# Optimization experiments

Measured on AMD Instinct MI355X. Metric: run time of the kernel, lower is better.

## Reference

```python
import jax, jax.numpy as jnp
import numpy as np

B, S, H = 256, 1024, 256  # batch, seq_len, hidden(==input_size)


def setup_inputs() -> dict:
    key = jax.random.key(0)
    ks = jax.random.split(key, 7)
    s = 1.0 / np.sqrt(H).astype(np.float32)
    return {
        "x": jax.random.normal(ks[0], (B, S, H), jnp.float32),
        "h_n": jax.random.normal(ks[1], (1, B, H), jnp.float32),
        "c_n": jax.random.normal(ks[2], (1, B, H), jnp.float32),
        "W_ih": jax.random.uniform(ks[3], (4 * H, H), jnp.float32, -s, s),
        "W_hh": jax.random.uniform(ks[4], (4 * H, H), jnp.float32, -s, s),
        "b_ih": jax.random.uniform(ks[5], (4 * H,), jnp.float32, -s, s),
        "b_hh": jax.random.uniform(ks[6], (4 * H,), jnp.float32, -s, s),
    }


def _lstm_decode(x, h_n, c_n, W_ih, W_hh, b_ih, b_hh):
    # Original torch loop: step 0 consumes h_n as the input token, step i>=1
    # consumes x[:, i-1]; outputs[:, i] is the hidden state after step i.
    h0, c0 = h_n[0], c_n[0]                               # (B, H)
    seq_in = jnp.concatenate([h0[:, None, :], x[:, :-1, :]], axis=1)  # (B, S, H)
    # Precompute input projections for the whole sequence (gate order i,f,g,o).
    x_proj = jnp.einsum("bsd,gd->bsg", seq_in, W_ih) + (b_ih + b_hh)   # (B, S, 4H)
    x_proj = jnp.swapaxes(x_proj, 0, 1)                   # (S, B, 4H)

    def step(carry, xp):
        h, c = carry
        gates = xp + h @ W_hh.T                           # (B, 4H)
        i, f, g, o = jnp.split(gates, 4, axis=-1)
        c = jax.nn.sigmoid(f) * c + jax.nn.sigmoid(i) * jnp.tanh(g)
        h = jax.nn.sigmoid(o) * jnp.tanh(c)
        return (h, c), h

    _, hs = jax.lax.scan(step, (h0, c0), x_proj)          # hs: (S, B, H)
    return jnp.swapaxes(hs, 0, 1)                         # (B, S, H)


def reference(x, h_n, c_n, W_ih, W_hh, b_ih, b_hh):
    return _lstm_decode(x, h_n, c_n, W_ih, W_hh, b_ih, b_hh)
```

## Files before the change

### kernel.cpp

```cpp
#include <hip/hip_runtime.h>
#include <stdint.h>


using bf16x8 = __attribute__((ext_vector_type(8))) __bf16;
using f32x4  = __attribute__((ext_vector_type(4))) float;
using u32x4  = __attribute__((ext_vector_type(4))) uint32_t;
using u16x2  = __attribute__((ext_vector_type(2))) uint16_t;

#define NCHUNK 8

#define XS_OFF   0ull
#define XS_SZ    134217728ull
#define WIH_OFF  (XS_OFF + XS_SZ)
#define W_SZ     524288ull
#define WHH_OFF  (WIH_OFF + W_SZ)
#define XP0_OFF  (WHH_OFF + W_SZ)
#define XP_SZ    67108864ull
#define XP1_OFF  (XP0_OFF + XP_SZ)
#define HST_OFF  (XP1_OFF + XP_SZ)
#define HST_SZ   131072ull
#define CST_OFF  (HST_OFF + HST_SZ)
#define CST_SZ   262144ull
#define BIAS_OFF (CST_OFF + CST_SZ)

#define WLDS_PER_WAVE 18432
#define HOFF   147456
#define LDS_BYTES 163840

#define SC_IFO -1.442695041f
#define SC_G   -2.885390082f

__device__ __forceinline__ uint16_t f2bf(float f) {
  uint32_t x = __float_as_uint(f);
  x += 0x7fffu + ((x >> 16) & 1u);
  return (uint16_t)(x >> 16);
}
__device__ __forceinline__ float bf2f(uint16_t u) {
  return __uint_as_float(((uint32_t)u) << 16);
}
__device__ __forceinline__ float frcp(float x) { return __builtin_amdgcn_rcpf(x); }
__device__ __forceinline__ float exp2a(float x) {
  float r; asm("v_exp_f32 %0, %1" : "=v"(r) : "v"(x)); return r;
}

__device__ __forceinline__ f32x4 mfma16(u32x4 a, u32x4 b, f32x4 c) {
  return __builtin_amdgcn_mfma_f32_16x16x32_bf16(
      __builtin_bit_cast(bf16x8, a), __builtin_bit_cast(bf16x8, b), c, 0, 0, 0);
}

#define W_IN_REG(f, kt) ((kt) < 5 || ((kt) == 5 && (f) < 6))
#define WIDX(f, kt)     ((f) < 6 ? (f) * 6 + (kt) : 36 + ((f) - 6) * 5 + (kt))
#define LIDX(f, kt)     ((kt) == 5 ? ((f) - 6) : ((kt) == 6 ? 2 + (f) : 10 + (f)))

__global__ __launch_bounds__(256) void pack_x_k(const float* __restrict__ x,
                                                const float* __restrict__ hn,
                                                uint16_t* __restrict__ xsp) {
  __shared__ uint16_t tile[64 * 256];
  const int t = blockIdx.x;
  const int tid = threadIdx.x;
  for (int pass = 0; pass < 2; ++pass) {
    const int r = tid >> 2;
    const int qq = tid & 3;
    const int rg = t * 128 + pass * 64 + r;
    const int s = rg >> 8, b = rg & 255;
    const float* src = s ? (x + ((size_t)b * 1024 + (s - 1)) * 256)
                         : (hn + (size_t)b * 256);
#pragma unroll
    for (int i = 0; i < 64; i += 2) {
      float2 v = *(const float2*)(src + qq * 64 + i);
      uint32_t kb = (uint32_t)(qq * 64 + i) * 2u;
      uint32_t addr = (uint32_t)r * 512u + (kb ^ (((uint32_t)r & 7u) << 4));
      u16x2 pr; pr.x = f2bf(v.x); pr.y = f2bf(v.y);
      *(u16x2*)((char*)tile + addr) = pr;
    }
    __syncthreads();
#pragma unroll
    for (int ff = 0; ff < 8; ++ff) {
      int task = ff * 256 + tid;
      int frag = task >> 6, lam = task & 63;
      int mt = frag >> 3, kt = frag & 7;
      int row = mt * 16 + (lam & 15);
      uint32_t kb = (uint32_t)(kt * 64 + (lam >> 4) * 16);
      u32x4 d = *(const u32x4*)((const char*)tile + row * 512 +
                                (kb ^ (((uint32_t)row & 7u) << 4)));
      size_t m16 = (size_t)t * 8 + pass * 4 + mt;
      *(u32x4*)(xsp + ((m16 * 8 + kt) * 64 + lam) * 8) = d;
    }
    __syncthreads();
  }
}

__global__ __launch_bounds__(256) void pack_misc_k(
    const float* __restrict__ wih, const float* __restrict__ whh,
    const float* __restrict__ bih, const float* __restrict__ bhh,
    const float* __restrict__ hn, const float* __restrict__ cn,
    uint16_t* __restrict__ wihp, uint16_t* __restrict__ whhp,
    float* __restrict__ bias, uint16_t* __restrict__ hst, float* __restrict__ cst) {
  const int blk = blockIdx.x, tid = threadIdx.x;
  if (blk < 32) {
    __shared__ uint16_t tile[64 * 256];
    const float* W = (blk < 16) ? wih : whh;
    uint16_t* WP = (blk < 16) ? wihp : whhp;
    const int rowbase = (blk & 15) * 64;
    const int r = tid >> 2, qq = tid & 3;
    const int n = rowbase + r;
    const float sc = ((n >> 8) == 2) ? SC_G : SC_IFO;
    const float* src = W + (size_t)n * 256;
#pragma unroll
    for (int i = 0; i < 64; i += 2) {
      float2 v = *(const float2*)(src + qq * 64 + i);
      uint32_t kb = (uint32_t)(qq * 64 + i) * 2u;
      uint32_t addr = (uint32_t)r * 512u + (kb ^ (((uint32_t)r & 7u) << 4));
      u16x2 pr; pr.x = f2bf(v.x * sc); pr.y = f2bf(v.y * sc);
      *(u16x2*)((char*)tile + addr) = pr;
    }
    __syncthreads();
#pragma unroll
    for (int ff = 0; ff < 8; ++ff) {
      int task = ff * 256 + tid;
      int frag = task >> 6, lam = task & 63;
      int mt = frag >> 3, kt = frag & 7;
      int row = mt * 16 + (lam & 15);
      uint32_t kb = (uint32_t)(kt * 64 + (lam >> 4) * 16);
      u32x4 d = *(const u32x4*)((const char*)tile + row * 512 +
                                (kb ^ (((uint32_t)row & 7u) << 4)));
      size_t nt = (size_t)(blk & 15) * 4 + mt;
      *(u32x4*)(WP + ((nt * 8 + kt) * 64 + lam) * 8) = d;
    }
  } else if (blk == 32) {
    for (int i = tid; i < 4096; i += 256) {
      float sc = ((i >> 8) == 2) ? SC_G : SC_IFO;
      bias[i] = (bih[i] + bhh[i]) * sc;
    }
  } else if (blk == 33) {
    for (int it = 0; it < 32; ++it) {
      int task = it * 256 + tid;
      int lam = task & 63;
      int kt = (task >> 6) & 7;
      int lb = task >> 9;
      int b = lb * 16 + (lam & 15);
      int k0 = kt * 32 + (lam >> 4) * 8;
      union { uint16_t s[8]; u32x4 v; } u;
#pragma unroll
      for (int j = 0; j < 8; ++j) u.s[j] = f2bf(hn[(size_t)b * 256 + k0 + j]);
      *(u32x4*)(hst + (size_t)task * 8) = u.v;
    }
  } else {
    for (int it = 0; it < 16; ++it) {
      int lt = it * 512 + (blk - 34) * 256 + tid;
      int l = lt & 63;
      int w = (lt >> 6) & 7;
      int lb = lt >> 9;
#pragma unroll
      for (int v = 0; v < 8; ++v) {
        int q = v & 3, hs = v >> 2;
        int bb = lb * 16 + (l >> 4) * 4 + q;
        int j = w * 32 + hs * 16 + (l & 15);
        cst[(size_t)lt * 8 + v] = cn[(size_t)bb * 256 + j];
      }
    }
  }
}

__global__ __launch_bounds__(512, 1) void fused_k(
    const uint16_t* __restrict__ xsp, const uint16_t* __restrict__ wihp,
    const uint16_t* __restrict__ whhp, const float* __restrict__ bias,
    uint16_t* __restrict__ xp0, uint16_t* __restrict__ xp1,
    uint16_t* __restrict__ hst, float* __restrict__ cst,
    float* __restrict__ out, int lstm_chunk, int gemm_chunk) {
  extern __shared__ __align__(16) char lds[];
  const int tid = threadIdx.x;
  const int l = tid & 63;
  const int w = tid >> 6;

  if (blockIdx.x < 16) {
    if (lstm_chunk < 0) return;
    const int c = lstm_chunk;
    const int blk = blockIdx.x;
    const uint16_t* __restrict__ xp = (c & 1) ? xp1 : xp0;

    u32x4 wr[46];
#pragma unroll
    for (int f = 0; f < 8; ++f) {
#pragma unroll
      for (int kt = 0; kt < 8; ++kt) {
        int nt = (f & 3) * 16 + (w * 2 + (f >> 2));
        u32x4 d = *(const u32x4*)(whhp + (((size_t)nt * 8 + kt) * 64 + l) * 8);
        if (W_IN_REG(f, kt))
          wr[WIDX(f, kt)] = d;
        else
          *(u32x4*)(lds + w * WLDS_PER_WAVE + LIDX(f, kt) * 1024 + l * 16) = d;
      }
    }
    *(u32x4*)(lds + HOFF + tid * 16) =
        *(const u32x4*)(hst + (size_t)blk * 4096 + (size_t)tid * 8);
    float creg[8];
    {
      const float* cs = cst + ((size_t)(blk * 8 + w) * 64 + l) * 8;
#pragma unroll
      for (int v = 0; v < 8; ++v) creg[v] = cs[v];
    }
    const char* xpbase = (const char*)xp +
        ((((size_t)blk * 128) * 16 + (size_t)(w * 2)) * 64 + l) * 32;
    float* ob = out + ((size_t)(blk * 16 + (l >> 4) * 4) * 1024 + (size_t)c * 128) * 256 + (l & 15);
    __syncthreads();

    int p = 0;
#pragma unroll 1
    for (int s = 0; s < 128; ++s) {
      const char* xc = xpbase + (size_t)s * 32768;
      union XV { uint16_t sv[16]; u32x4 v[2]; };
      XV xv0;
      xv0.v[0] = *(const u32x4*)(xc);
      xv0.v[1] = *(const u32x4*)(xc + 16);
      const char* hb = lds + HOFF + p * 8192 + l * 16;
      char* hw = lds + HOFF + (p ^ 1) * 8192;

      f32x4 acc0[4] = {};
#pragma unroll
      for (int kt = 0; kt < 8; ++kt) {
        u32x4 a = *(const u32x4*)(hb + kt * 1024);
#pragma unroll
        for (int g = 0; g < 4; ++g) {
          u32x4 b = W_IN_REG(g, kt)
                        ? wr[WIDX(g, kt)]
                        : *(const u32x4*)(lds + w * WLDS_PER_WAVE + LIDX(g, kt) * 1024 + l * 16);
          acc0[g] = mfma16(a, b, acc0[g]);
        }
      }
      XV xv1;
      xv1.v[0] = *(const u32x4*)(xc + 2048);
      xv1.v[1] = *(const u32x4*)(xc + 2048 + 16);
      {
        const int j = (w * 2) * 16 + (l & 15);
        char* hwj = hw + (j >> 5) * 1024 + (((j >> 3) & 3) * 16) * 16 + (j & 7) * 2;
        float* obh = ob + (size_t)s * 256 + (w * 2) * 16;
#pragma unroll
        for (int q = 0; q < 4; ++q) {
          float xi = acc0[0][q] + bf2f(xv0.sv[0 * 4 + q]);
          float xf = acc0[1][q] + bf2f(xv0.sv[1 * 4 + q]);
          float xg = acc0[2][q] + bf2f(xv0.sv[2 * 4 + q]);
          float xo = acc0[3][q] + bf2f(xv0.sv[3 * 4 + q]);
          float I = frcp(1.f + exp2a(xi));
          float F = frcp(1.f + exp2a(xf));
          float T = fmaf(2.f, frcp(1.f + exp2a(xg)), -1.f);
          float O = frcp(1.f + exp2a(xo));
          float cv = fmaf(F, creg[q], I * T);
          creg[q] = cv;
          float th = fmaf(2.f, frcp(1.f + exp2a(SC_G * cv)), -1.f);
          float hv = O * th;
          obh[(size_t)q * 262144] = hv;
          int m = (l >> 4) * 4 + q;
          *(uint16_t*)(hwj + m * 16) = f2bf(hv);
        }
      }

      f32x4 acc1[4] = {};
#pragma unroll
      for (int kt = 0; kt < 8; ++kt) {
        u32x4 a = *(const u32x4*)(hb + kt * 1024);
#pragma unroll
        for (int g = 0; g < 4; ++g) {
          u32x4 b = W_IN_REG(4 + g, kt)
                        ? wr[WIDX(4 + g, kt)]
                        : *(const u32x4*)(lds + w * WLDS_PER_WAVE + LIDX(4 + g, kt) * 1024 + l * 16);
          acc1[g] = mfma16(a, b, acc1[g]);
        }
      }
      {
        const int j = (w * 2 + 1) * 16 + (l & 15);
        char* hwj = hw + (j >> 5) * 1024 + (((j >> 3) & 3) * 16) * 16 + (j & 7) * 2;
        float* obh = ob + (size_t)s * 256 + (w * 2 + 1) * 16;
#pragma unroll
        for (int q = 0; q < 4; ++q) {
          float xi = acc1[0][q] + bf2f(xv1.sv[0 * 4 + q]);
          float xf = acc1[1][q] + bf2f(xv1.sv[1 * 4 + q]);
          float xg = acc1[2][q] + bf2f(xv1.sv[2 * 4 + q]);
          float xo = acc1[3][q] + bf2f(xv1.sv[3 * 4 + q]);
          float I = frcp(1.f + exp2a(xi));
          float F = frcp(1.f + exp2a(xf));
          float T = fmaf(2.f, frcp(1.f + exp2a(xg)), -1.f);
          float O = frcp(1.f + exp2a(xo));
          float cv = fmaf(F, creg[4 + q], I * T);
          creg[4 + q] = cv;
          float th = fmaf(2.f, frcp(1.f + exp2a(SC_G * cv)), -1.f);
          float hv = O * th;
          obh[(size_t)q * 262144] = hv;
          int m = (l >> 4) * 4 + q;
          *(uint16_t*)(hwj + m * 16) = f2bf(hv);
        }
      }
      __syncthreads();
      p ^= 1;
    }
    *(u32x4*)(hst + (size_t)blk * 4096 + (size_t)tid * 8) =
        *(const u32x4*)(lds + HOFF + p * 8192 + tid * 16);
    {
      float* cs = cst + ((size_t)(blk * 8 + w) * 64 + l) * 8;
#pragma unroll
      for (int v = 0; v < 8; ++v) cs[v] = creg[v];
    }
    return;
  }

  if (gemm_chunk < 0) return;
  const int c = gemm_chunk;
  const int bid = blockIdx.x - 16;
  const int sg = bid >> 4;
  const int bb = bid & 15;

  f32x4 acc[4][2][4] = {};
#pragma unroll
  for (int kt = 0; kt < 8; ++kt) {
    u32x4 av[4];
#pragma unroll
    for (int mt = 0; mt < 4; ++mt) {
      size_t m16 = (size_t)(c * 128 + sg * 4 + mt) * 16 + bb;
      av[mt] = *(const u32x4*)(xsp + ((m16 * 8 + kt) * 64 + l) * 8);
    }
    u32x4 bv[2][4];
#pragma unroll
    for (int jj = 0; jj < 2; ++jj)
#pragma unroll
      for (int g = 0; g < 4; ++g) {
        size_t nt = (size_t)(g * 16 + w * 2 + jj);
        bv[jj][g] = *(const u32x4*)(wihp + ((nt * 8 + kt) * 64 + l) * 8);
      }
#pragma unroll
    for (int mt = 0; mt < 4; ++mt)
#pragma unroll
      for (int jj = 0; jj < 2; ++jj)
#pragma unroll
        for (int g = 0; g < 4; ++g)
          acc[mt][jj][g] = mfma16(av[mt], bv[jj][g], acc[mt][jj][g]);
  }
  uint16_t* __restrict__ xpo = (c & 1) ? xp1 : xp0;
  float badd[2][4];
#pragma unroll
  for (int jj = 0; jj < 2; ++jj)
#pragma unroll
    for (int g = 0; g < 4; ++g)
      badd[jj][g] = bias[(g * 16 + w * 2 + jj) * 16 + (l & 15)];
#pragma unroll
  for (int mt = 0; mt < 4; ++mt)
#pragma unroll
    for (int jj = 0; jj < 2; ++jj) {
      union { uint16_t s[16]; u32x4 v[2]; } pk;
#pragma unroll
      for (int g = 0; g < 4; ++g)
#pragma unroll
        for (int q = 0; q < 4; ++q)
          pk.s[g * 4 + q] = f2bf(acc[mt][jj][g][q] + badd[jj][g]);
      size_t cell = ((size_t)bb * 128 + (size_t)(sg * 4 + mt)) * 16 + (size_t)(w * 2 + jj);
      char* dst = (char*)xpo + cell * 2048 + (size_t)l * 32;
      *(u32x4*)dst = pk.v[0];
      *(u32x4*)(dst + 16) = pk.v[1];
    }
}

extern "C" void kernel_launch(void* const* d_in, const int* in_sizes, int n_in,
                              void* d_out, int out_size, void* d_ws, size_t ws_size,
                              hipStream_t stream) {
  const float* x   = (const float*)d_in[0];
  const float* hn  = (const float*)d_in[1];
  const float* cn  = (const float*)d_in[2];
  const float* wih = (const float*)d_in[3];
  const float* whh = (const float*)d_in[4];
  const float* bih = (const float*)d_in[5];
  const float* bhh = (const float*)d_in[6];
  float* out = (float*)d_out;
  char* ws = (char*)d_ws;

  uint16_t* xsp  = (uint16_t*)(ws + XS_OFF);
  uint16_t* wihp = (uint16_t*)(ws + WIH_OFF);
  uint16_t* whhp = (uint16_t*)(ws + WHH_OFF);
  uint16_t* xp0  = (uint16_t*)(ws + XP0_OFF);
  uint16_t* xp1  = (uint16_t*)(ws + XP1_OFF);
  uint16_t* hst  = (uint16_t*)(ws + HST_OFF);
  float*    cst  = (float*)(ws + CST_OFF);
  float*    bias = (float*)(ws + BIAS_OFF);

  hipFuncSetAttribute(reinterpret_cast<const void*>(fused_k),
                      hipFuncAttributeMaxDynamicSharedMemorySize, LDS_BYTES);

  hipLaunchKernelGGL(pack_x_k, dim3(2048), dim3(256), 0, stream, x, hn, xsp);
  hipLaunchKernelGGL(pack_misc_k, dim3(36), dim3(256), 0, stream,
                     wih, whh, bih, bhh, hn, cn, wihp, whhp, bias, hst, cst);
  for (int c = 0; c <= NCHUNK; ++c) {
    int lc = c - 1;
    int gc = (c < NCHUNK) ? c : -1;
    hipLaunchKernelGGL(fused_k, dim3(528), dim3(512), LDS_BYTES, stream,
                       xsp, wihp, whhp, bias, xp0, xp1, hst, cst, out, lc, gc);
  }
}
```

Before: 2.689 ms.

## Split LSTM recurrence across 64 blocks with cross-block flag synchronization

Result: slower. 8.001 ms (+197.5%).

```diff
diff --git a/kernel.cpp b/kernel.cpp
--- a/kernel.cpp
+++ b/kernel.cpp
@@ -5,6 +5,7 @@
 using bf16x8 = __attribute__((ext_vector_type(8))) __bf16;
 using f32x4  = __attribute__((ext_vector_type(4))) float;
 using u32x4  = __attribute__((ext_vector_type(4))) uint32_t;
+using u32x2  = __attribute__((ext_vector_type(2))) uint32_t;
 using u16x2  = __attribute__((ext_vector_type(2))) uint16_t;
 
 #define NCHUNK 8
@@ -17,15 +18,18 @@
 #define XP0_OFF  (WHH_OFF + W_SZ)
 #define XP_SZ    67108864ull
 #define XP1_OFF  (XP0_OFF + XP_SZ)
-#define HST_OFF  (XP1_OFF + XP_SZ)
-#define HST_SZ   131072ull
-#define CST_OFF  (HST_OFF + HST_SZ)
+#define HX_OFF   (XP1_OFF + XP_SZ)
+#define HX_SZ    262144ull
+#define FLG_OFF  (HX_OFF + HX_SZ)
+#define FLG_SZ   4096ull
+#define CST_OFF  (FLG_OFF + FLG_SZ)
 #define CST_SZ   262144ull
 #define BIAS_OFF (CST_OFF + CST_SZ)
 
-#define WLDS_PER_WAVE 18432
-#define HOFF   147456
-#define LDS_BYTES 163840
+#define HBUF_OFF 0
+#define GBUF_OFF 8192
+#define STG_OFF  24576
+#define LDS_BYTES 98304
 
 #define SC_IFO -1.442695041f
 #define SC_G   -2.885390082f
@@ -42,15 +46,16 @@
 __device__ __forceinline__ float exp2a(float x) {
   float r; asm("v_exp_f32 %0, %1" : "=v"(r) : "v"(x)); return r;
 }
-
 __device__ __forceinline__ f32x4 mfma16(u32x4 a, u32x4 b, f32x4 c) {
   return __builtin_amdgcn_mfma_f32_16x16x32_bf16(
       __builtin_bit_cast(bf16x8, a), __builtin_bit_cast(bf16x8, b), c, 0, 0, 0);
 }
-
-#define W_IN_REG(f, kt) ((kt) < 5 || ((kt) == 5 && (f) < 6))
-#define WIDX(f, kt)     ((f) < 6 ? (f) * 6 + (kt) : 36 + ((f) - 6) * 5 + (kt))
-#define LIDX(f, kt)     ((kt) == 5 ? ((f) - 6) : ((kt) == 6 ? 2 + (f) : 10 + (f)))
+__device__ __forceinline__ uint32_t flag_ld(const uint32_t* p) {
+  return __hip_atomic_load(p, __ATOMIC_ACQUIRE, __HIP_MEMORY_SCOPE_AGENT);
+}
+__device__ __forceinline__ void flag_st(uint32_t* p, uint32_t v) {
+  __hip_atomic_store(p, v, __ATOMIC_RELEASE, __HIP_MEMORY_SCOPE_AGENT);
+}
 
 __global__ __launch_bounds__(256) void pack_x_k(const float* __restrict__ x,
                                                 const float* __restrict__ hn,
@@ -95,7 +100,8 @@
     const float* __restrict__ bih, const float* __restrict__ bhh,
     const float* __restrict__ hn, const float* __restrict__ cn,
     uint16_t* __restrict__ wihp, uint16_t* __restrict__ whhp,
-    float* __restrict__ bias, uint16_t* __restrict__ hst, float* __restrict__ cst) {
+    float* __restrict__ bias, char* __restrict__ hx,
+    uint32_t* __restrict__ flags, float* __restrict__ cst) {
   const int blk = blockIdx.x, tid = threadIdx.x;
   if (blk < 32) {
     __shared__ uint16_t tile[64 * 256];
@@ -132,180 +138,175 @@
       float sc = ((i >> 8) == 2) ? SC_G : SC_IFO;
       bias[i] = (bih[i] + bhh[i]) * sc;
     }
+    for (int i = tid; i < 1024; i += 256) flags[i] = 0u;
   } else if (blk == 33) {
     for (int it = 0; it < 32; ++it) {
-      int task = it * 256 + tid;
-      int lam = task & 63;
-      int kt = (task >> 6) & 7;
-      int lb = task >> 9;
-      int b = lb * 16 + (lam & 15);
-      int k0 = kt * 32 + (lam >> 4) * 8;
+      int item = it * 256 + tid;
+      int lane = item & 63;
+      int ktl = (item >> 6) & 1;
+      int slice = item >> 7;
+      int g = slice >> 2, ns = slice & 3;
+      int b = g * 16 + (lane & 15);
+      int k0 = ns * 64 + ktl * 32 + (lane >> 4) * 8;
       union { uint16_t s[8]; u32x4 v; } u;
 #pragma unroll
-      for (int j = 0; j < 8; ++j) u.s[j] = f2bf(hn[(size_t)b * 256 + k0 + j]);
-      *(u32x4*)(hst + (size_t)task * 8) = u.v;
+      for (int e = 0; e < 8; ++e) u.s[e] = f2bf(hn[(size_t)b * 256 + k0 + e]);
+      *(u32x4*)(hx + (size_t)slice * 2048 + ktl * 1024 + lane * 16) = u.v;
     }
   } else {
-    for (int it = 0; it < 16; ++it) {
-      int lt = it * 512 + (blk - 34) * 256 + tid;
-      int l = lt & 63;
-      int w = (lt >> 6) & 7;
-      int lb = lt >> 9;
-#pragma unroll
-      for (int v = 0; v < 8; ++v) {
-        int q = v & 3, hs = v >> 2;
-        int bb = lb * 16 + (l >> 4) * 4 + q;
-        int j = w * 32 + hs * 16 + (l & 15);
-        cst[(size_t)lt * 8 + v] = cn[(size_t)bb * 256 + j];
-      }
-    }
-  }
-}
-
-__global__ __launch_bounds__(512, 1) void fused_k(
+    for (int it = 0; it < 128; ++it) {
+      int idx = (blk - 34) * 32768 + it * 256 + tid;
+      int slice = idx >> 10, ci = idx & 1023;
+      int g = slice >> 2, ns = slice & 3;
+      int b = g * 16 + (ci >> 6);
+      int j = ns * 64 + (ci & 63);
+      cst[idx] = cn[(size_t)b * 256 + j];
+    }
+  }
+}
+
+__global__ __launch_bounds__(512) void fused_k(
     const uint16_t* __restrict__ xsp, const uint16_t* __restrict__ wihp,
     const uint16_t* __restrict__ whhp, const float* __restrict__ bias,
     uint16_t* __restrict__ xp0, uint16_t* __restrict__ xp1,
-    uint16_t* __restrict__ hst, float* __restrict__ cst,
-    float* __restrict__ out, int lstm_chunk, int gemm_chunk) {
+    char* __restrict__ hx, uint32_t* __restrict__ flags,
+    float* __restrict__ cst, float* __restrict__ out,
+    int lstm_chunk, int gemm_chunk) {
   extern __shared__ __align__(16) char lds[];
   const int tid = threadIdx.x;
   const int l = tid & 63;
   const int w = tid >> 6;
 
-  if (blockIdx.x < 16) {
+  if (blockIdx.x < 64) {
     if (lstm_chunk < 0) return;
     const int c = lstm_chunk;
-    const int blk = blockIdx.x;
+    const uint32_t cb = (uint32_t)(c * 128);
+    const int slice = blockIdx.x;
+    const int g = slice >> 2, ns = slice & 3;
     const uint16_t* __restrict__ xp = (c & 1) ? xp1 : xp0;
-
-    u32x4 wr[46];
-#pragma unroll
-    for (int f = 0; f < 8; ++f) {
+    char* hbuf = lds + HBUF_OFF;
+    float* gbuf = (float*)(lds + GBUF_OFF);
+    char* stg = lds + STG_OFF;
+
+    u32x4 wr0[8], wr1[8];
+    {
+      int nl0 = 2 * w, nl1 = 2 * w + 1;
+      int ng0 = (nl0 >> 2) * 16 + ns * 4 + (nl0 & 3);
+      int ng1 = (nl1 >> 2) * 16 + ns * 4 + (nl1 & 3);
 #pragma unroll
       for (int kt = 0; kt < 8; ++kt) {
-        int nt = (f & 3) * 16 + (w * 2 + (f >> 2));
-        u32x4 d = *(const u32x4*)(whhp + (((size_t)nt * 8 + kt) * 64 + l) * 8);
-        if (W_IN_REG(f, kt))
-          wr[WIDX(f, kt)] = d;
-        else
-          *(u32x4*)(lds + w * WLDS_PER_WAVE + LIDX(f, kt) * 1024 + l * 16) = d;
-      }
-    }
-    *(u32x4*)(lds + HOFF + tid * 16) =
-        *(const u32x4*)(hst + (size_t)blk * 4096 + (size_t)tid * 8);
-    float creg[8];
-    {
-      const float* cs = cst + ((size_t)(blk * 8 + w) * 64 + l) * 8;
-#pragma unroll
-      for (int v = 0; v < 8; ++v) creg[v] = cs[v];
-    }
-    const char* xpbase = (const char*)xp +
-        ((((size_t)blk * 128) * 16 + (size_t)(w * 2)) * 64 + l) * 32;
-    float* ob = out + ((size_t)(blk * 16 + (l >> 4) * 4) * 1024 + (size_t)c * 128) * 256 + (l & 15);
-    __syncthreads();
-
-    int p = 0;
+        wr0[kt] = *(const u32x4*)(whhp + (((size_t)ng0 * 8 + kt) * 64 + l) * 8);
+        wr1[kt] = *(const u32x4*)(whhp + (((size_t)ng1 * 8 + kt) * 64 + l) * 8);
+      }
+    }
+    float cc0 = cst[(size_t)slice * 1024 + tid];
+    float cc1 = cst[(size_t)slice * 1024 + tid + 512];
+
+    int m0 = tid >> 6, jl0 = tid & 63;
+    int m1 = (tid + 512) >> 6, jl1 = jl0;
+    float* gp0 = gbuf + (jl0 >> 4) * 256 + m0 * 16 + (jl0 & 15);
+    float* gp1 = gbuf + (jl1 >> 4) * 256 + m1 * 16 + (jl1 & 15);
+    char* sp0 = stg + (jl0 >> 5) * 1024 + (((jl0 & 31) >> 3) * 16 + m0) * 16 + (jl0 & 7) * 2;
+    char* sp1 = stg + (jl1 >> 5) * 1024 + (((jl1 & 31) >> 3) * 16 + m1) * 16 + (jl1 & 7) * 2;
+    float* op0 = out + ((size_t)(g * 16 + m0) * 1024 + (size_t)c * 128) * 256 + ns * 64 + jl0;
+    float* op1 = out + ((size_t)(g * 16 + m1) * 1024 + (size_t)c * 128) * 256 + ns * 64 + jl1;
+    const char* xpb = (const char*)xp + (size_t)slice * 1048576 + (size_t)(2 * w) * 512 + (size_t)l * 8;
+    float* gb0 = gbuf + (2 * w) * 256 + ((l >> 4) * 4) * 16 + (l & 15);
+    float* gb1 = gb0 + 256;
+
+    if (w == 0) {
+      const char* src = hx + (size_t)slice * 2048 + (size_t)l * 32;
+      u32x4 d0 = *(const u32x4*)src;
+      u32x4 d1 = *(const u32x4*)(src + 16);
+      *(u32x4*)(hbuf + ns * 2048 + l * 32) = d0;
+      *(u32x4*)(hbuf + ns * 2048 + l * 32 + 16) = d1;
+    }
+
 #pragma unroll 1
     for (int s = 0; s < 128; ++s) {
-      const char* xc = xpbase + (size_t)s * 32768;
-      union XV { uint16_t sv[16]; u32x4 v[2]; };
-      XV xv0;
-      xv0.v[0] = *(const u32x4*)(xc);
-      xv0.v[1] = *(const u32x4*)(xc + 16);
-      const char* hb = lds + HOFF + p * 8192 + l * 16;
-      char* hw = lds + HOFF + (p ^ 1) * 8192;
-
-      f32x4 acc0[4] = {};
-#pragma unroll
-      for (int kt = 0; kt < 8; ++kt) {
-        u32x4 a = *(const u32x4*)(hb + kt * 1024);
-#pragma unroll
-        for (int g = 0; g < 4; ++g) {
-          u32x4 b = W_IN_REG(g, kt)
-                        ? wr[WIDX(g, kt)]
-                        : *(const u32x4*)(lds + w * WLDS_PER_WAVE + LIDX(g, kt) * 1024 + l * 16);
-          acc0[g] = mfma16(a, b, acc0[g]);
+      if (w >= 1 && w < 4) {
+        const int nsr = (ns + w) & 3;
+        const uint32_t tgt = cb + (uint32_t)s;
+        if (l == 0) {
+          while (flag_ld(&flags[(g * 4 + nsr) * 16]) < tgt)
+            __builtin_amdgcn_s_sleep(2);
         }
-      }
-      XV xv1;
-      xv1.v[0] = *(const u32x4*)(xc + 2048);
-      xv1.v[1] = *(const u32x4*)(xc + 2048 + 16);
+        const char* src = hx + (size_t)(s & 1) * 131072 +
+                          (size_t)(g * 4 + nsr) * 2048 + (size_t)l * 32;
+        u32x4 d0 = *(const u32x4*)src;
+        u32x4 d1 = *(const u32x4*)(src + 16);
+        *(u32x4*)(hbuf + nsr * 2048 + l * 32) = d0;
+        *(u32x4*)(hbuf + nsr * 2048 + l * 32 + 16) = d1;
+      }
+      __syncthreads();
+
       {
-        const int j = (w * 2) * 16 + (l & 15);
-        char* hwj = hw + (j >> 5) * 1024 + (((j >> 3) & 3) * 16) * 16 + (j & 7) * 2;
-        float* obh = ob + (size_t)s * 256 + (w * 2) * 16;
+        const char* xc = xpb + (size_t)s * 8192;
+        union { uint16_t sv[4]; u32x2 v; } xv0, xv1;
+        xv0.v = *(const u32x2*)(xc);
+        xv1.v = *(const u32x2*)(xc + 512);
+        f32x4 acc0 = {}, acc1 = {};
+#pragma unroll
+        for (int kt = 0; kt < 8; ++kt) {
+          u32x4 a = *(const u32x4*)(hbuf + kt * 1024 + l * 16);
+          acc0 = mfma16(a, wr0[kt], acc0);
+          acc1 = mfma16(a, wr1[kt], acc1);
+        }
 #pragma unroll
         for (int q = 0; q < 4; ++q) {
-          float xi = acc0[0][q] + bf2f(xv0.sv[0 * 4 + q]);
-          float xf = acc0[1][q] + bf2f(xv0.sv[1 * 4 + q]);
-          float xg = acc0[2][q] + bf2f(xv0.sv[2 * 4 + q]);
-          float xo = acc0[3][q] + bf2f(xv0.sv[3 * 4 + q]);
-          float I = frcp(1.f + exp2a(xi));
-          float F = frcp(1.f + exp2a(xf));
-          float T = fmaf(2.f, frcp(1.f + exp2a(xg)), -1.f);
-          float O = frcp(1.f + exp2a(xo));
-          float cv = fmaf(F, creg[q], I * T);
-          creg[q] = cv;
-          float th = fmaf(2.f, frcp(1.f + exp2a(SC_G * cv)), -1.f);
-          float hv = O * th;
-          obh[(size_t)q * 262144] = hv;
-          int m = (l >> 4) * 4 + q;
-          *(uint16_t*)(hwj + m * 16) = f2bf(hv);
+          gb0[q * 16] = acc0[q] + bf2f(xv0.sv[q]);
+          gb1[q * 16] = acc1[q] + bf2f(xv1.sv[q]);
         }
       }
-
-      f32x4 acc1[4] = {};
-#pragma unroll
-      for (int kt = 0; kt < 8; ++kt) {
-        u32x4 a = *(const u32x4*)(hb + kt * 1024);
-#pragma unroll
-        for (int g = 0; g < 4; ++g) {
-          u32x4 b = W_IN_REG(4 + g, kt)
-                        ? wr[WIDX(4 + g, kt)]
-                        : *(const u32x4*)(lds + w * WLDS_PER_WAVE + LIDX(4 + g, kt) * 1024 + l * 16);
-          acc1[g] = mfma16(a, b, acc1[g]);
-        }
-      }
+      __syncthreads();
+
       {
-        const int j = (w * 2 + 1) * 16 + (l & 15);
-        char* hwj = hw + (j >> 5) * 1024 + (((j >> 3) & 3) * 16) * 16 + (j & 7) * 2;
-        float* obh = ob + (size_t)s * 256 + (w * 2 + 1) * 16;
-#pragma unroll
-        for (int q = 0; q < 4; ++q) {
-          float xi = acc1[0][q] + bf2f(xv1.sv[0 * 4 + q]);
-          float xf = acc1[1][q] + bf2f(xv1.sv[1 * 4 + q]);
-          float xg = acc1[2][q] + bf2f(xv1.sv[2 * 4 + q]);
-          float xo = acc1[3][q] + bf2f(xv1.sv[3 * 4 + q]);
-          float I = frcp(1.f + exp2a(xi));
-          float F = frcp(1.f + exp2a(xf));
-          float T = fmaf(2.f, frcp(1.f + exp2a(xg)), -1.f);
-          float O = frcp(1.f + exp2a(xo));
-          float cv = fmaf(F, creg[4 + q], I * T);
-          creg[4 + q] = cv;
-          float th = fmaf(2.f, frcp(1.f + exp2a(SC_G * cv)), -1.f);
-          float hv = O * th;
-          obh[(size_t)q * 262144] = hv;
-          int m = (l >> 4) * 4 + q;
-          *(uint16_t*)(hwj + m * 16) = f2bf(hv);
-        }
+        float xi = gp0[0], xf = gp0[1024], xg = gp0[2048], xo = gp0[3072];
+        float I = frcp(1.f + exp2a(xi));
+        float F = frcp(1.f + exp2a(xf));
+        float T = fmaf(2.f, frcp(1.f + exp2a(xg)), -1.f);
+        float O = frcp(1.f + exp2a(xo));
+        float cv = fmaf(F, cc0, I * T);
+        cc0 = cv;
+        float hv = O * fmaf(2.f, frcp(1.f + exp2a(SC_G * cv)), -1.f);
+        op0[(size_t)s * 256] = hv;
+        *(uint16_t*)sp0 = f2bf(hv);
+      }
+      {
+        float xi = gp1[0], xf = gp1[1024], xg = gp1[2048], xo = gp1[3072];
+        float I = frcp(1.f + exp2a(xi));
+        float F = frcp(1.f + exp2a(xf));
+        float T = fmaf(2.f, frcp(1.f + exp2a(xg)), -1.f);
+        float O = frcp(1.f + exp2a(xo));
+        float cv = fmaf(F, cc1, I * T);
+        cc1 = cv;
+        float hv = O * fmaf(2.f, frcp(1.f + exp2a(SC_G * cv)), -1.f);
+        op1[(size_t)s * 256] = hv;
+        *(uint16_t*)sp1 = f2bf(hv);
       }
       __syncthreads();
-      p ^= 1;
-    }
-    *(u32x4*)(hst + (size_t)blk * 4096 + (size_t)tid * 8) =
-        *(const u32x4*)(lds + HOFF + p * 8192 + tid * 16);
-    {
-      float* cs = cst + ((size_t)(blk * 8 + w) * 64 + l) * 8;
-#pragma unroll
-      for (int v = 0; v < 8; ++v) cs[v] = creg[v];
-    }
+
+      if (w == 0) {
+        u32x4 s0 = *(const u32x4*)(stg + l * 32);
+        u32x4 s1 = *(const u32x4*)(stg + l * 32 + 16);
+        char* dst = hx + (size_t)((s + 1) & 1) * 131072 +
+                    (size_t)slice * 2048 + (size_t)l * 32;
+        *(u32x4*)dst = s0;
+        *(u32x4*)(dst + 16) = s1;
+        *(u32x4*)(hbuf + ns * 2048 + l * 32) = s0;
+        *(u32x4*)(hbuf + ns * 2048 + l * 32 + 16) = s1;
+        __threadfence();
+        if (l == 0) flag_st(&flags[slice * 16], cb + (uint32_t)(s + 1));
+      }
+    }
+    cst[(size_t)slice * 1024 + tid] = cc0;
+    cst[(size_t)slice * 1024 + tid + 512] = cc1;
     return;
   }
 
   if (gemm_chunk < 0) return;
-  const int c = gemm_chunk;
-  const int bid = blockIdx.x - 16;
+  const int cg = gemm_chunk;
+  const int bid = blockIdx.x - 64;
   const int sg = bid >> 4;
   const int bb = bid & 15;
 
@@ -315,46 +316,48 @@
     u32x4 av[4];
 #pragma unroll
     for (int mt = 0; mt < 4; ++mt) {
-      size_t m16 = (size_t)(c * 128 + sg * 4 + mt) * 16 + bb;
+      size_t m16 = (size_t)(cg * 128 + sg * 4 + mt) * 16 + bb;
       av[mt] = *(const u32x4*)(xsp + ((m16 * 8 + kt) * 64 + l) * 8);
     }
     u32x4 bv[2][4];
 #pragma unroll
     for (int jj = 0; jj < 2; ++jj)
 #pragma unroll
-      for (int g = 0; g < 4; ++g) {
-        size_t nt = (size_t)(g * 16 + w * 2 + jj);
-        bv[jj][g] = *(const u32x4*)(wihp + ((nt * 8 + kt) * 64 + l) * 8);
+      for (int gi = 0; gi < 4; ++gi) {
+        size_t nt = (size_t)(gi * 16 + w * 2 + jj);
+        bv[jj][gi] = *(const u32x4*)(wihp + ((nt * 8 + kt) * 64 + l) * 8);
       }
 #pragma unroll
     for (int mt = 0; mt < 4; ++mt)
 #pragma unroll
       for (int jj = 0; jj < 2; ++jj)
 #pragma unroll
-        for (int g = 0; g < 4; ++g)
-          acc[mt][jj][g] = mfma16(av[mt], bv[jj][g], acc[mt][jj][g]);
-  }
-  uint16_t* __restrict__ xpo = (c & 1) ? xp1 : xp0;
+        for (int gi = 0; gi < 4; ++gi)
+          acc[mt][jj][gi] = mfma16(av[mt], bv[jj][gi], acc[mt][jj][gi]);
+  }
+  uint16_t* __restrict__ xpo = (cg & 1) ? xp1 : xp0;
   float badd[2][4];
 #pragma unroll
   for (int jj = 0; jj < 2; ++jj)
 #pragma unroll
-    for (int g = 0; g < 4; ++g)
-      badd[jj][g] = bias[(g * 16 + w * 2 + jj) * 16 + (l & 15)];
+    for (int gi = 0; gi < 4; ++gi)
+      badd[jj][gi] = bias[(gi * 16 + w * 2 + jj) * 16 + (l & 15)];
 #pragma unroll
   for (int mt = 0; mt < 4; ++mt)
 #pragma unroll
     for (int jj = 0; jj < 2; ++jj) {
-      union { uint16_t s[16]; u32x4 v[2]; } pk;
-#pragma unroll
-      for (int g = 0; g < 4; ++g)
+      int ntt = w * 2 + jj;
+      int slicex = bb * 4 + (ntt >> 2);
+      int jt = ntt & 3;
+      int s_loc = sg * 4 + mt;
+#pragma unroll
+      for (int gi = 0; gi < 4; ++gi) {
+        union { uint16_t sv[4]; u32x2 v; } pk;
 #pragma unroll
         for (int q = 0; q < 4; ++q)
-          pk.s[g * 4 + q] = f2bf(acc[mt][jj][g][q] + badd[jj][g]);
-      size_t cell = ((size_t)bb * 128 + (size_t)(sg * 4 + mt)) * 16 + (size_t)(w * 2 + jj);
-      char* dst = (char*)xpo + cell * 2048 + (size_t)l * 32;
-      *(u32x4*)dst = pk.v[0];
-      *(u32x4*)(dst + 16) = pk.v[1];
+          pk.sv[q] = f2bf(acc[mt][jj][gi][q] + badd[jj][gi]);
+        *(u32x2*)(xpo + ((((size_t)slicex * 128 + s_loc) * 16 + gi * 4 + jt) * 64 + l) * 4) = pk.v;
+      }
     }
 }
 
@@ -371,25 +374,26 @@
   float* out = (float*)d_out;
   char* ws = (char*)d_ws;
 
-  uint16_t* xsp  = (uint16_t*)(ws + XS_OFF);
-  uint16_t* wihp = (uint16_t*)(ws + WIH_OFF);
-  uint16_t* whhp = (uint16_t*)(ws + WHH_OFF);
-  uint16_t* xp0  = (uint16_t*)(ws + XP0_OFF);
-  uint16_t* xp1  = (uint16_t*)(ws + XP1_OFF);
-  uint16_t* hst  = (uint16_t*)(ws + HST_OFF);
-  float*    cst  = (float*)(ws + CST_OFF);
-  float*    bias = (float*)(ws + BIAS_OFF);
+  uint16_t* xsp   = (uint16_t*)(ws + XS_OFF);
+  uint16_t* wihp  = (uint16_t*)(ws + WIH_OFF);
+  uint16_t* whhp  = (uint16_t*)(ws + WHH_OFF);
+  uint16_t* xp0   = (uint16_t*)(ws + XP0_OFF);
+  uint16_t* xp1   = (uint16_t*)(ws + XP1_OFF);
+  char*     hx    = ws + HX_OFF;
+  uint32_t* flags = (uint32_t*)(ws + FLG_OFF);
+  float*    cst   = (float*)(ws + CST_OFF);
+  float*    bias  = (float*)(ws + BIAS_OFF);
 
   hipFuncSetAttribute(reinterpret_cast<const void*>(fused_k),
                       hipFuncAttributeMaxDynamicSharedMemorySize, LDS_BYTES);
 
   hipLaunchKernelGGL(pack_x_k, dim3(2048), dim3(256), 0, stream, x, hn, xsp);
   hipLaunchKernelGGL(pack_misc_k, dim3(36), dim3(256), 0, stream,
-                     wih, whh, bih, bhh, hn, cn, wihp, whhp, bias, hst, cst);
+                     wih, whh, bih, bhh, hn, cn, wihp, whhp, bias, hx, flags, cst);
   for (int c = 0; c <= NCHUNK; ++c) {
     int lc = c - 1;
     int gc = (c < NCHUNK) ? c : -1;
-    hipLaunchKernelGGL(fused_k, dim3(528), dim3(512), LDS_BYTES, stream,
-                       xsp, wihp, whhp, bias, xp0, xp1, hst, cst, out, lc, gc);
-  }
-}
+    hipLaunchKernelGGL(fused_k, dim3(576), dim3(512), LDS_BYTES, stream,
+                       xsp, wihp, whhp, bias, xp0, xp1, hx, flags, cst, out, lc, gc);
+  }
+}
```

## Halve LSTM block width to 4 waves with 96 register-resident weight tiles

Applied to the files above, without the earlier changes.

Result: slower. 4.085 ms (+51.9%).

```diff
diff --git a/kernel.cpp b/kernel.cpp
--- a/kernel.cpp
+++ b/kernel.cpp
@@ -5,6 +5,7 @@
 using bf16x8 = __attribute__((ext_vector_type(8))) __bf16;
 using f32x4  = __attribute__((ext_vector_type(4))) float;
 using u32x4  = __attribute__((ext_vector_type(4))) uint32_t;
+using u32x2  = __attribute__((ext_vector_type(2))) uint32_t;
 using u16x2  = __attribute__((ext_vector_type(2))) uint16_t;
 
 #define NCHUNK 8
@@ -23,9 +24,9 @@
 #define CST_SZ   262144ull
 #define BIAS_OFF (CST_OFF + CST_SZ)
 
-#define WLDS_PER_WAVE 18432
-#define HOFF   147456
-#define LDS_BYTES 163840
+#define WLDS_PER_WAVE 32768
+#define HOFF   131072
+#define LDS_BYTES 147456
 
 #define SC_IFO -1.442695041f
 #define SC_G   -2.885390082f
@@ -42,15 +43,10 @@
 __device__ __forceinline__ float exp2a(float x) {
   float r; asm("v_exp_f32 %0, %1" : "=v"(r) : "v"(x)); return r;
 }
-
 __device__ __forceinline__ f32x4 mfma16(u32x4 a, u32x4 b, f32x4 c) {
   return __builtin_amdgcn_mfma_f32_16x16x32_bf16(
       __builtin_bit_cast(bf16x8, a), __builtin_bit_cast(bf16x8, b), c, 0, 0, 0);
 }
-
-#define W_IN_REG(f, kt) ((kt) < 5 || ((kt) == 5 && (f) < 6))
-#define WIDX(f, kt)     ((f) < 6 ? (f) * 6 + (kt) : 36 + ((f) - 6) * 5 + (kt))
-#define LIDX(f, kt)     ((kt) == 5 ? ((f) - 6) : ((kt) == 6 ? 2 + (f) : 10 + (f)))
 
 __global__ __launch_bounds__(256) void pack_x_k(const float* __restrict__ x,
                                                 const float* __restrict__ hn,
@@ -146,23 +142,24 @@
       *(u32x4*)(hst + (size_t)task * 8) = u.v;
     }
   } else {
-    for (int it = 0; it < 16; ++it) {
-      int lt = it * 512 + (blk - 34) * 256 + tid;
-      int l = lt & 63;
-      int w = (lt >> 6) & 7;
-      int lb = lt >> 9;
-#pragma unroll
-      for (int v = 0; v < 8; ++v) {
-        int q = v & 3, hs = v >> 2;
-        int bb = lb * 16 + (l >> 4) * 4 + q;
-        int j = w * 32 + hs * 16 + (l & 15);
-        cst[(size_t)lt * 8 + v] = cn[(size_t)bb * 256 + j];
-      }
-    }
-  }
-}
-
-__global__ __launch_bounds__(512, 1) void fused_k(
+    for (int it = 0; it < 128; ++it) {
+      int idx = (blk - 34) * 32768 + it * 256 + tid;
+      int v = idx & 15;
+      int lq = (idx >> 4) & 63;
+      int ww = (idx >> 10) & 3;
+      int lb = idx >> 12;
+      int h = v >> 3, jt = (v >> 2) & 1, q = v & 3;
+      int b = lb * 16 + (lq >> 4) * 4 + q;
+      int j = (ww * 4 + h * 2 + jt) * 16 + (lq & 15);
+      cst[idx] = cn[(size_t)b * 256 + j];
+    }
+  }
+}
+
+__global__
+__attribute__((amdgpu_flat_work_group_size(256, 256)))
+__attribute__((amdgpu_waves_per_eu(1, 1)))
+void fused_k(
     const uint16_t* __restrict__ xsp, const uint16_t* __restrict__ wihp,
     const uint16_t* __restrict__ whhp, const float* __restrict__ bias,
     uint16_t* __restrict__ xp0, uint16_t* __restrict__ xp1,
@@ -178,184 +175,174 @@
     const int c = lstm_chunk;
     const int blk = blockIdx.x;
     const uint16_t* __restrict__ xp = (c & 1) ? xp1 : xp0;
-
-    u32x4 wr[46];
-#pragma unroll
-    for (int f = 0; f < 8; ++f) {
+    char* wl = lds + w * WLDS_PER_WAVE;
+
+    u32x4 wr[96];
+#pragma unroll
+    for (int fi = 0; fi < 16; ++fi) {
+      int g = fi & 3, hj = fi >> 2;
+      int nt = g * 16 + w * 4 + hj;
 #pragma unroll
       for (int kt = 0; kt < 8; ++kt) {
-        int nt = (f & 3) * 16 + (w * 2 + (f >> 2));
         u32x4 d = *(const u32x4*)(whhp + (((size_t)nt * 8 + kt) * 64 + l) * 8);
-        if (W_IN_REG(f, kt))
-          wr[WIDX(f, kt)] = d;
+        if (kt < 2)
+          *(u32x4*)(wl + fi * 2048 + kt * 1024 + l * 16) = d;
         else
-          *(u32x4*)(lds + w * WLDS_PER_WAVE + LIDX(f, kt) * 1024 + l * 16) = d;
+          wr[fi * 6 + (kt - 2)] = d;
       }
     }
-    *(u32x4*)(lds + HOFF + tid * 16) =
-        *(const u32x4*)(hst + (size_t)blk * 4096 + (size_t)tid * 8);
-    float creg[8];
+    float creg[16];
     {
-      const float* cs = cst + ((size_t)(blk * 8 + w) * 64 + l) * 8;
-#pragma unroll
-      for (int v = 0; v < 8; ++v) creg[v] = cs[v];
-    }
-    const char* xpbase = (const char*)xp +
-        ((((size_t)blk * 128) * 16 + (size_t)(w * 2)) * 64 + l) * 32;
+      const float* cs = cst + ((size_t)(blk * 4 + w) * 64 + l) * 16;
+#pragma unroll
+      for (int v = 0; v < 16; ++v) creg[v] = cs[v];
+    }
+    {
+      const char* src = (const char*)hst + (size_t)blk * 8192 + (size_t)tid * 32;
+      *(u32x4*)(lds + HOFF + tid * 32) = *(const u32x4*)src;
+      *(u32x4*)(lds + HOFF + tid * 32 + 16) = *(const u32x4*)(src + 16);
+    }
+    const char* xpb = (const char*)xp +
+        ((((size_t)blk * 128) * 4 + w) * 2) * 4096 + (size_t)l * 64;
     float* ob = out + ((size_t)(blk * 16 + (l >> 4) * 4) * 1024 + (size_t)c * 128) * 256 + (l & 15);
     __syncthreads();
+
+    union XV { uint16_t sv[32]; u32x4 v[4]; };
 
     int p = 0;
 #pragma unroll 1
     for (int s = 0; s < 128; ++s) {
-      const char* xc = xpbase + (size_t)s * 32768;
-      union XV { uint16_t sv[16]; u32x4 v[2]; };
+      const char* hb = lds + HOFF + p * 8192 + l * 16;
+      char* hw = lds + HOFF + (p ^ 1) * 8192;
+      const char* xc = xpb + (size_t)s * 32768;
+
+      auto do_half = [&](int half, XV& xv) {
+        f32x4 acc[2][4] = {};
+#pragma unroll
+        for (int kt = 0; kt < 8; ++kt) {
+          u32x4 a = *(const u32x4*)(hb + kt * 1024);
+#pragma unroll
+          for (int jt = 0; jt < 2; ++jt)
+#pragma unroll
+            for (int g = 0; g < 4; ++g) {
+              int fi = (half * 2 + jt) * 4 + g;
+              u32x4 b = (kt < 2)
+                  ? *(const u32x4*)(wl + fi * 2048 + kt * 1024 + l * 16)
+                  : wr[fi * 6 + (kt - 2)];
+              acc[jt][g] = mfma16(a, b, acc[jt][g]);
+            }
+        }
+#pragma unroll
+        for (int jt = 0; jt < 2; ++jt) {
+          const int j = (w * 4 + half * 2 + jt) * 16 + (l & 15);
+          char* hwj = hw + (j >> 5) * 1024 + ((j >> 3) & 3) * 256 +
+                      (l >> 4) * 64 + (j & 7) * 2;
+          float* obh = ob + (size_t)s * 256 + (w * 4 + half * 2 + jt) * 16;
+#pragma unroll
+          for (int q = 0; q < 4; ++q) {
+            float xi = acc[jt][0][q] + bf2f(xv.sv[0 * 8 + jt * 4 + q]);
+            float xf = acc[jt][1][q] + bf2f(xv.sv[1 * 8 + jt * 4 + q]);
+            float xg = acc[jt][2][q] + bf2f(xv.sv[2 * 8 + jt * 4 + q]);
+            float xo = acc[jt][3][q] + bf2f(xv.sv[3 * 8 + jt * 4 + q]);
+            float I = frcp(1.f + exp2a(xi));
+            float F = frcp(1.f + exp2a(xf));
+            float T = fmaf(2.f, frcp(1.f + exp2a(xg)), -1.f);
+            float O = frcp(1.f + exp2a(xo));
+            int ci = half * 8 + jt * 4 + q;
+            float cv = fmaf(F, creg[ci], I * T);
+            creg[ci] = cv;
+            float hv = O * fmaf(2.f, frcp(1.f + exp2a(SC_G * cv)), -1.f);
+            obh[(size_t)q * 262144] = hv;
+            *(uint16_t*)(hwj + q * 16) = f2bf(hv);
+          }
+        }
+      };
+
       XV xv0;
       xv0.v[0] = *(const u32x4*)(xc);
       xv0.v[1] = *(const u32x4*)(xc + 16);
-      const char* hb = lds + HOFF + p * 8192 + l * 16;
-      char* hw = lds + HOFF + (p ^ 1) * 8192;
-
-      f32x4 acc0[4] = {};
-#pragma unroll
-      for (int kt = 0; kt < 8; ++kt) {
-        u32x4 a = *(const u32x4*)(hb + kt * 1024);
+      xv0.v[2] = *(const u32x4*)(xc + 32);
+      xv0.v[3] = *(const u32x4*)(xc + 48);
+      do_half(0, xv0);
+      XV xv1;
+      xv1.v[0] = *(const u32x4*)(xc + 4096);
+      xv1.v[1] = *(const u32x4*)(xc + 4096 + 16);
+      xv1.v[2] = *(const u32x4*)(xc + 4096 + 32);
+      xv1.v[3] = *(const u32x4*)(xc + 4096 + 48);
+      do_half(1, xv1);
+      __syncthreads();
+      p ^= 1;
+    }
+    {
+      const char* src = lds + HOFF + p * 8192 + tid * 32;
+      char* dst = (char*)hst + (size_t)blk * 8192 + (size_t)tid * 32;
+      *(u32x4*)dst = *(const u32x4*)src;
+      *(u32x4*)(dst + 16) = *(const u32x4*)(src + 16);
+      float* cs = cst + ((size_t)(blk * 4 + w) * 64 + l) * 16;
+#pragma unroll
+      for (int v = 0; v < 16; ++v) cs[v] = creg[v];
+    }
+    return;
+  }
+
+  if (gemm_chunk < 0) return;
+  const int cg = gemm_chunk;
+  const int bid = blockIdx.x - 16;
+  const int bb = bid & 15;
+  const int st = bid >> 4;
+  uint16_t* __restrict__ xpo = (cg & 1) ? xp1 : xp0;
+
+  float badd[4][4];
+#pragma unroll
+  for (int g = 0; g < 4; ++g)
+#pragma unroll
+    for (int jj = 0; jj < 4; ++jj)
+      badd[g][jj] = bias[(g * 16 + w * 4 + jj) * 16 + (l & 15)];
+
+#pragma unroll 1
+  for (int pr = 0; pr < 4; ++pr) {
+    f32x4 acc[2][16] = {};
+#pragma unroll
+    for (int kt = 0; kt < 8; ++kt) {
+      u32x4 av[2];
+#pragma unroll
+      for (int t = 0; t < 2; ++t) {
+        size_t m16 = (size_t)(cg * 128 + st * 8 + pr * 2 + t) * 16 + bb;
+        av[t] = *(const u32x4*)(xsp + ((m16 * 8 + kt) * 64 + l) * 8);
+      }
+      u32x4 bv[16];
+#pragma unroll
+      for (int fi = 0; fi < 16; ++fi) {
+        int g = fi >> 2, jj = fi & 3;
+        size_t nt = (size_t)(g * 16 + w * 4 + jj);
+        bv[fi] = *(const u32x4*)(wihp + ((nt * 8 + kt) * 64 + l) * 8);
+      }
+#pragma unroll
+      for (int t = 0; t < 2; ++t)
+#pragma unroll
+        for (int fi = 0; fi < 16; ++fi)
+          acc[t][fi] = mfma16(av[t], bv[fi], acc[t][fi]);
+    }
+#pragma unroll
+    for (int t = 0; t < 2; ++t) {
+      int s = st * 8 + pr * 2 + t;
+#pragma unroll
+      for (int jj = 0; jj < 4; ++jj) {
+        int half = jj >> 1, jt = jj & 1;
+        char* dst = (char*)xpo +
+            ((((size_t)bb * 128 + s) * 4 + w) * 2 + half) * 4096 +
+            (size_t)l * 64 + jt * 8;
 #pragma unroll
         for (int g = 0; g < 4; ++g) {
-          u32x4 b = W_IN_REG(g, kt)
-                        ? wr[WIDX(g, kt)]
-                        : *(const u32x4*)(lds + w * WLDS_PER_WAVE + LIDX(g, kt) * 1024 + l * 16);
-          acc0[g] = mfma16(a, b, acc0[g]);
+          union { uint16_t sv[4]; u32x2 v2; } pk;
+#pragma unroll
+          for (int q = 0; q < 4; ++q)
+            pk.sv[q] = f2bf(acc[t][g * 4 + jj][q] + badd[g][jj]);
+          *(u32x2*)(dst + g * 16) = pk.v2;
         }
       }
-      XV xv1;
-      xv1.v[0] = *(const u32x4*)(xc + 2048);
-      xv1.v[1] = *(const u32x4*)(xc + 2048 + 16);
-      {
-        const int j = (w * 2) * 16 + (l & 15);
-        char* hwj = hw + (j >> 5) * 1024 + (((j >> 3) & 3) * 16) * 16 + (j & 7) * 2;
-        float* obh = ob + (size_t)s * 256 + (w * 2) * 16;
-#pragma unroll
-        for (int q = 0; q < 4; ++q) {
-          float xi = acc0[0][q] + bf2f(xv0.sv[0 * 4 + q]);
-          float xf = acc0[1][q] + bf2f(xv0.sv[1 * 4 + q]);
-          float xg = acc0[2][q] + bf2f(xv0.sv[2 * 4 + q]);
-          float xo = acc0[3][q] + bf2f(xv0.sv[3 * 4 + q]);
-          float I = frcp(1.f + exp2a(xi));
-          float F = frcp(1.f + exp2a(xf));
-          float T = fmaf(2.f, frcp(1.f + exp2a(xg)), -1.f);
-          float O = frcp(1.f + exp2a(xo));
-          float cv = fmaf(F, creg[q], I * T);
-          creg[q] = cv;
-          float th = fmaf(2.f, frcp(1.f + exp2a(SC_G * cv)), -1.f);
-          float hv = O * th;
-          obh[(size_t)q * 262144] = hv;
-          int m = (l >> 4) * 4 + q;
-          *(uint16_t*)(hwj + m * 16) = f2bf(hv);
-        }
-      }
-
-      f32x4 acc1[4] = {};
-#pragma unroll
-      for (int kt = 0; kt < 8; ++kt) {
-        u32x4 a = *(const u32x4*)(hb + kt * 1024);
-#pragma unroll
-        for (int g = 0; g < 4; ++g) {
-          u32x4 b = W_IN_REG(4 + g, kt)
-                        ? wr[WIDX(4 + g, kt)]
-                        : *(const u32x4*)(lds + w * WLDS_PER_WAVE + LIDX(4 + g, kt) * 1024 + l * 16);
-          acc1[g] = mfma16(a, b, acc1[g]);
-        }
-      }
-      {
-        const int j = (w * 2 + 1) * 16 + (l & 15);
-        char* hwj = hw + (j >> 5) * 1024 + (((j >> 3) & 3) * 16) * 16 + (j & 7) * 2;
-        float* obh = ob + (size_t)s * 256 + (w * 2 + 1) * 16;
-#pragma unroll
-        for (int q = 0; q < 4; ++q) {
-          float xi = acc1[0][q] + bf2f(xv1.sv[0 * 4 + q]);
-          float xf = acc1[1][q] + bf2f(xv1.sv[1 * 4 + q]);
-          float xg = acc1[2][q] + bf2f(xv1.sv[2 * 4 + q]);
-          float xo = acc1[3][q] + bf2f(xv1.sv[3 * 4 + q]);
-          float I = frcp(1.f + exp2a(xi));
-          float F = frcp(1.f + exp2a(xf));
-          float T = fmaf(2.f, frcp(1.f + exp2a(xg)), -1.f);
-          float O = frcp(1.f + exp2a(xo));
-          float cv = fmaf(F, creg[4 + q], I * T);
-          creg[4 + q] = cv;
-          float th = fmaf(2.f, frcp(1.f + exp2a(SC_G * cv)), -1.f);
-          float hv = O * th;
-          obh[(size_t)q * 262144] = hv;
-          int m = (l >> 4) * 4 + q;
-          *(uint16_t*)(hwj + m * 16) = f2bf(hv);
-        }
-      }
-      __syncthreads();
-      p ^= 1;
-    }
-    *(u32x4*)(hst + (size_t)blk * 4096 + (size_t)tid * 8) =
-        *(const u32x4*)(lds + HOFF + p * 8192 + tid * 16);
-    {
-      float* cs = cst + ((size_t)(blk * 8 + w) * 64 + l) * 8;
-#pragma unroll
-      for (int v = 0; v < 8; ++v) cs[v] = creg[v];
-    }
-    return;
-  }
-
-  if (gemm_chunk < 0) return;
-  const int c = gemm_chunk;
-  const int bid = blockIdx.x - 16;
-  const int sg = bid >> 4;
-  const int bb = bid & 15;
-
-  f32x4 acc[4][2][4] = {};
-#pragma unroll
-  for (int kt = 0; kt < 8; ++kt) {
-    u32x4 av[4];
-#pragma unroll
-    for (int mt = 0; mt < 4; ++mt) {
-      size_t m16 = (size_t)(c * 128 + sg * 4 + mt) * 16 + bb;
-      av[mt] = *(const u32x4*)(xsp + ((m16 * 8 + kt) * 64 + l) * 8);
-    }
-    u32x4 bv[2][4];
-#pragma unroll
-    for (int jj = 0; jj < 2; ++jj)
-#pragma unroll
-      for (int g = 0; g < 4; ++g) {
-        size_t nt = (size_t)(g * 16 + w * 2 + jj);
-        bv[jj][g] = *(const u32x4*)(wihp + ((nt * 8 + kt) * 64 + l) * 8);
-      }
-#pragma unroll
-    for (int mt = 0; mt < 4; ++mt)
-#pragma unroll
-      for (int jj = 0; jj < 2; ++jj)
-#pragma unroll
-        for (int g = 0; g < 4; ++g)
-          acc[mt][jj][g] = mfma16(av[mt], bv[jj][g], acc[mt][jj][g]);
-  }
-  uint16_t* __restrict__ xpo = (c & 1) ? xp1 : xp0;
-  float badd[2][4];
-#pragma unroll
-  for (int jj = 0; jj < 2; ++jj)
-#pragma unroll
-    for (int g = 0; g < 4; ++g)
-      badd[jj][g] = bias[(g * 16 + w * 2 + jj) * 16 + (l & 15)];
-#pragma unroll
-  for (int mt = 0; mt < 4; ++mt)
-#pragma unroll
-    for (int jj = 0; jj < 2; ++jj) {
-      union { uint16_t s[16]; u32x4 v[2]; } pk;
-#pragma unroll
-      for (int g = 0; g < 4; ++g)
-#pragma unroll
-        for (int q = 0; q < 4; ++q)
-          pk.s[g * 4 + q] = f2bf(acc[mt][jj][g][q] + badd[jj][g]);
-      size_t cell = ((size_t)bb * 128 + (size_t)(sg * 4 + mt)) * 16 + (size_t)(w * 2 + jj);
-      char* dst = (char*)xpo + cell * 2048 + (size_t)l * 32;
-      *(u32x4*)dst = pk.v[0];
-      *(u32x4*)(dst + 16) = pk.v[1];
-    }
+    }
+  }
 }
 
 extern "C" void kernel_launch(void* const* d_in, const int* in_sizes, int n_in,
@@ -389,7 +376,7 @@
   for (int c = 0; c <= NCHUNK; ++c) {
     int lc = c - 1;
     int gc = (c < NCHUNK) ? c : -1;
-    hipLaunchKernelGGL(fused_k, dim3(528), dim3(512), LDS_BYTES, stream,
+    hipLaunchKernelGGL(fused_k, dim3(272), dim3(256), LDS_BYTES, stream,
                        xsp, wihp, whhp, bias, xp0, xp1, hst, cst, out, lc, gc);
   }
 }
```
